# Optimization experiments

Measured on AMD Instinct MI355X. Metric: run time of the kernel, lower is better.

Reference implementation:

```python
import jax, jax.numpy as jnp
import numpy as np

B, S = 64, 100
N_EX, N_Q = 3000, 128
N_AT, N_IT = 1000, 1000
D_A = D_E = D_K = 128
GAMMA = 0.03


def _xavier(k, shape):
    lim = float(np.sqrt(6.0 / (shape[0] + shape[1])))
    return jax.random.uniform(k, shape, jnp.float32, -lim, lim)


def setup_inputs() -> dict:
    key = jax.random.key(0)
    ks = jax.random.split(key, 20)
    nq1 = N_Q + 1
    e_data = jax.random.randint(ks[0], (B, S), 0, N_EX, dtype=jnp.int32)
    a_data = jax.random.randint(ks[1], (B, S), 0, 2, dtype=jnp.int32)
    it_data = jax.random.randint(ks[2], (B, S), 0, N_IT, dtype=jnp.int32)
    at_data = jax.random.randint(ks[3], (B, S), 0, N_AT, dtype=jnp.int32)
    # binary Q-matrix with zeros replaced by gamma (as done in LPKT.__init__)
    q_bin = (jax.random.uniform(ks[4], (N_EX + 10, nq1)) < 0.05).astype(jnp.float32)
    q_matrix = jnp.where(q_bin > 0, 1.0, GAMMA)
    E_at = _xavier(ks[5], (N_AT + 10, D_K))
    E_it = _xavier(ks[6], (N_IT + 10, D_K))
    E_e = _xavier(ks[7], (N_EX + 10, D_E))
    h0 = _xavier(ks[8], (nq1, D_K))  # xavier-initialized initial skill state
    W1 = _xavier(ks[9], (D_A + D_E + D_K, D_K)); b1 = jnp.zeros(D_K, jnp.float32)
    W2 = _xavier(ks[10], (4 * D_K, D_K)); b2 = jnp.zeros(D_K, jnp.float32)
    W3 = _xavier(ks[11], (4 * D_K, D_K)); b3 = jnp.zeros(D_K, jnp.float32)
    W4 = _xavier(ks[12], (3 * D_K, D_K)); b4 = jnp.zeros(D_K, jnp.float32)
    W5 = _xavier(ks[13], (D_E + D_K, D_K)); b5 = jnp.zeros(D_K, jnp.float32)
    return dict(e_data=e_data, a_data=a_data, it_data=it_data, at_data=at_data,
                q_matrix=q_matrix, h0=h0, E_e=E_e, E_at=E_at, E_it=E_it,
                W1=W1, b1=b1, W2=W2, b2=b2, W3=W3, b3=b3, W4=W4, b4=b4, W5=W5, b5=b5)


def reference(e_data, a_data, it_data, at_data, q_matrix, h0, E_e, E_at, E_it,
              W1, b1, W2, b2, W3, b3, W4, b4, W5, b5):
    Bv, Sv = e_data.shape
    d_k = W2.shape[1]
    d_a = W1.shape[0] - E_e.shape[1] - d_k
    e_emb = E_e[e_data]            # (B,S,d_e)
    at_emb = E_at[at_data]         # (B,S,d_k)
    it_emb = E_it[it_data]         # (B,S,d_k)
    a_rep = jnp.broadcast_to(a_data.astype(jnp.float32)[..., None], (Bv, Sv, d_a))
    all_learning = jnp.concatenate([e_emb, at_emb, a_rep], 2) @ W1 + b1  # (B,S,d_k)
    q_all = q_matrix[e_data]       # (B,S,nq1)
    h_pre0 = jnp.broadcast_to(h0, (Bv,) + h0.shape)  # (B,nq1,d_k)
    q0 = q_all[:, 0]
    ht0 = jnp.einsum('bn,bnd->bd', q0, h_pre0) / q0.sum(1, keepdims=True)
    W4h, W4l, W4i = jnp.split(W4, 3, axis=0)

    def step(carry, x):
        learning_pre, h_pre, h_tilde_pre = carry
        q_e, q_next, it, learning, e_next = x
        feat = jnp.concatenate([learning_pre, it, learning, h_tilde_pre], 1)  # (B,4dk)
        lg = jnp.tanh(feat @ W2 + b2)
        gamma_l = jax.nn.sigmoid(feat @ W3 + b3)
        LG = gamma_l * (lg + 1.0) * 0.5                       # (B,d_k)
        LG_tilde = q_e[:, :, None] * LG[:, None, :]           # (B,nq1,d_k); dropout=eval identity
        gamma_f = jax.nn.sigmoid(jnp.einsum('bnd,df->bnf', h_pre, W4h)
                                 + (LG @ W4l + it @ W4i + b4)[:, None, :])
        h = LG_tilde + gamma_f * h_pre
        h_tilde = jnp.einsum('bn,bnd->bd', q_next, h) / q_next.sum(1, keepdims=True)
        y = jax.nn.sigmoid(jnp.concatenate([e_next, h_tilde], 1) @ W5 + b5).sum(1) / d_k
        return (learning, h, h_tilde), y

    xs = (jnp.swapaxes(q_all[:, :-1], 0, 1), jnp.swapaxes(q_all[:, 1:], 0, 1),
          jnp.swapaxes(it_emb[:, :-1], 0, 1), jnp.swapaxes(all_learning[:, :-1], 0, 1),
          jnp.swapaxes(e_emb[:, 1:], 0, 1))
    learning_pre0 = jnp.zeros((Bv, d_k), jnp.float32)
    _, ys = jax.lax.scan(step, (learning_pre0, h_pre0, ht0), xs)  # ys: (S-1,B)
    pred = jnp.zeros((Bv, Sv), jnp.float32).at[:, 1:].set(ys.T)
    return pred
```

## Files before the change

kernel.cpp:

```cpp
#include <hip/hip_runtime.h>
#include <hip/hip_fp16.h>
#include <math.h>


#define BB   64
#define SS   100
#define DK   128
#define NTH  512

#define OFF_PW1AB   0
#define OFF_PW23ABC 16384
#define OFF_PW4I    65536
#define OFF_PW5A    73728
#define OFF_PW23D   81920
#define OFF_PW4L    98304
#define OFF_AFRAG   114688
#define OFF_S1      122880
#define OFF_AL      123008
#define OFF_PRE     532608
#define OFF_HTV     2171008

typedef __attribute__((ext_vector_type(16))) float floatx16;
typedef __attribute__((ext_vector_type(8)))  short short8v;
typedef __attribute__((ext_vector_type(2)))  float floatx2;

__device__ __forceinline__ float frcp(float x) { return __builtin_amdgcn_rcpf(x); }
__device__ __forceinline__ float fsig(float x) { float t = __expf(-x); return frcp(1.0f + t); }
__device__ __forceinline__ float ftanh(float x) {
    x = fminf(20.0f, fmaxf(-20.0f, x));
    float t = __expf(-2.0f * x);
    return (1.0f - t) * frcp(1.0f + t);
}
__device__ __forceinline__ unsigned bfbits(float x) {
    unsigned u = __float_as_uint(x);
    return (u + 0x7fffu + ((u >> 16) & 1u)) >> 16;
}
__device__ __forceinline__ unsigned pack2(float a, float b) {
    return bfbits(a) | (bfbits(b) << 16);
}
__device__ __forceinline__ float blo(unsigned u) { return __uint_as_float(u << 16); }
__device__ __forceinline__ float bhi(unsigned u) { return __uint_as_float(u & 0xffff0000u); }

__device__ __forceinline__ unsigned cvtpk(float a, float b) {
    unsigned r;
    asm("v_cvt_pk_bf16_f32 %0, %1, %2" : "=v"(r) : "v"(a), "v"(b));
    return r;
}

__device__ __forceinline__ void wg_barrier() {
    asm volatile("s_waitcnt lgkmcnt(0)" ::: "memory");
    __builtin_amdgcn_s_barrier();
    asm volatile("" ::: "memory");
}

__global__ void k0_prep(const float* __restrict__ W1, const float* __restrict__ W2,
                        const float* __restrict__ W3, const float* __restrict__ W4,
                        const float* __restrict__ W5, unsigned* __restrict__ ws) {
    int g = blockIdx.x * blockDim.x + threadIdx.x;
    if (g < 16384) {
        int s = g >> 7, d = g & 127;
        ws[OFF_PW1AB + g] = pack2(W1[(2*s)*DK + d], W1[(2*s+1)*DK + d]);
    } else if (g < 65536) {
        int i = g - 16384; int s = i >> 8, j = i & 255;
        const float* M = (j < 128) ? W2 : W3; int jj = j & 127;
        ws[g] = pack2(M[(2*s)*DK + jj], M[(2*s+1)*DK + jj]);
    } else if (g < 73728) {
        int i = g - 65536; int s = i >> 7, j = i & 127;
        ws[g] = pack2(W4[(256+2*s)*DK + j], W4[(257+2*s)*DK + j]);
    } else if (g < 81920) {
        int i = g - 73728; int s = i >> 7, j = i & 127;
        ws[g] = pack2(W5[(2*s)*DK + j], W5[(2*s+1)*DK + j]);
    } else if (g < 98304) {
        int i = g - 81920;
        int q = i & 3, ln = (i >> 2) & 63, kb = (i >> 8) & 7, cw = i >> 11;
        int k = 16*kb + 8*(ln >> 5) + 2*q;
        int j = 32*cw + (ln & 31);
        const float* M = (j < 128) ? W2 : W3; int jj = j & 127;
        ws[g] = pack2(M[(384+k)*DK + jj], M[(385+k)*DK + jj]);
    } else if (g < 106496) {
        int i = g - 98304;
        int q = i & 3, ln = (i >> 2) & 63, kb = (i >> 8) & 7, cw = i >> 11;
        int k = 16*kb + 8*(ln >> 5) + 2*q;
        int j = 32*cw + (ln & 31);
        ws[g] = pack2(W4[(128+k)*DK + j], W4[(129+k)*DK + j]);
    } else if (g < 114688) {
    } else if (g < 122880) {
        int i = g - 114688;
        int gg = i >> 11, kb = (i >> 8) & 7, ln = (i >> 2) & 63, c = i & 3;
        int m = ln & 31, hp = ln >> 5;
        int k0 = 16*kb + 8*hp + 2*c;
        ws[g] = pack2(W4[k0*DK + 32*gg + m], W4[(k0+1)*DK + 32*gg + m]);
    } else if (g < 123008) {
        int d = g - 122880;
        float z = 0.f;
        for (int k = 0; k < 128; k++) z += W1[(256+k)*DK + d];
        ws[g] = __float_as_uint(z);
    }
}

__global__ __launch_bounds__(128)
void k1_al(const int* __restrict__ e_data, const int* __restrict__ a_data,
           const int* __restrict__ at_data, const float* __restrict__ Ee,
           const float* __restrict__ Eat, const float* __restrict__ b1,
           unsigned* __restrict__ ws) {
    const int b = blockIdx.x, t0 = 4 * blockIdx.y, tid = threadIdx.x;
    __shared__ __align__(16) float s_f[4][256];
    #pragma unroll
    for (int r = 0; r < 8; r++) {
        int id = r * 128 + tid; int i = id >> 8, k = id & 255;
        int t = t0 + i; float v = 0.f;
        if (t <= 98) {
            int e  = e_data[b*SS + t];
            int at = at_data[b*SS + t];
            v = (k < 128) ? Ee[(size_t)e*DK + k] : Eat[(size_t)at*DK + (k-128)];
        }
        s_f[i][k] = v;
    }
    __syncthreads();
    float s1v = __uint_as_float(ws[OFF_S1 + tid]);
    float b1v = b1[tid];
    float z[4];
    #pragma unroll
    for (int i = 0; i < 4; i++) z[i] = 0.f;
    #pragma unroll 2
    for (int s = 0; s < 128; s++) {
        unsigned w = ws[OFF_PW1AB + s*128 + tid];
        float wl = blo(w), wh = bhi(w);
        #pragma unroll
        for (int i = 0; i < 4; i++) {
            float2 f = *(const float2*)&s_f[i][2*s];
            z[i] += f.x*wl + f.y*wh;
        }
    }
    __half* AL = (__half*)(ws + OFF_AL);
    #pragma unroll
    for (int i = 0; i < 4; i++) {
        int t = t0 + i;
        if (t <= 98) {
            float a = (float)a_data[b*SS + t];
            AL[(size_t)(b*SS + t)*DK + tid] = __float2half(z[i] + a*s1v + b1v);
        }
    }
}

__global__ __launch_bounds__(512)
void k2_pre(const int* __restrict__ e_data, const int* __restrict__ it_data,
            const float* __restrict__ Eit, const float* __restrict__ Ee,
            const float* __restrict__ b2, const float* __restrict__ b3,
            const float* __restrict__ b4, const float* __restrict__ b5,
            unsigned* __restrict__ ws) {
    const int b = blockIdx.x, t0 = 4 * blockIdx.y, tid = threadIdx.x;
    __shared__ __align__(16) float s_g[4][384];
    __shared__ __align__(16) float s_e[4][128];
    const __half* AL = (const __half*)(ws + OFF_AL);
    #pragma unroll
    for (int r = 0; r < 3; r++) {
        int id = r * 512 + tid; int i = id / 384; int k = id - 384*i;
        int t = t0 + i; float v = 0.f;
        if (t <= 98) {
            if (k < 128)      v = (t == 0) ? 0.f : (float)AL[(size_t)(b*SS + t - 1)*DK + k];
            else if (k < 256) v = Eit[(size_t)it_data[b*SS + t]*DK + (k - 128)];
            else              v = (float)AL[(size_t)(b*SS + t)*DK + (k - 256)];
        }
        s_g[i][k] = v;
    }
    {
        int id = tid; int i = id >> 7, k = id & 127;
        int t = t0 + i;
        s_e[i][k] = (t <= 98) ? Ee[(size_t)e_data[b*SS + t + 1]*DK + k] : 0.f;
    }
    __syncthreads();
    __half* PRE = (__half*)(ws + OFF_PRE);
    float z[4];
    #pragma unroll
    for (int i = 0; i < 4; i++) z[i] = 0.f;
    int col; float bb;
    if (tid < 256) {
        int j = tid;
        #pragma unroll 2
        for (int s = 0; s < 192; s++) {
            unsigned w = ws[OFF_PW23ABC + s*256 + j];
            float wl = blo(w), wh = bhi(w);
            #pragma unroll
            for (int i = 0; i < 4; i++) {
                float2 f = *(const float2*)&s_g[i][2*s];
                z[i] += f.x*wl + f.y*wh;
            }
        }
        col = j; bb = (j < 128) ? b2[j] : b3[j - 128];
    } else if (tid < 384) {
        int j = tid - 256;
        #pragma unroll 2
        for (int s = 0; s < 64; s++) {
            unsigned w = ws[OFF_PW4I + s*128 + j];
            float wl = blo(w), wh = bhi(w);
            #pragma unroll
            for (int i = 0; i < 4; i++) {
                float2 f = *(const float2*)&s_g[i][128 + 2*s];
                z[i] += f.x*wl + f.y*wh;
            }
        }
        col = 256 + j; bb = b4[j];
    } else {
        int j = tid - 384;
        #pragma unroll 2
        for (int s = 0; s < 64; s++) {
            unsigned w = ws[OFF_PW5A + s*128 + j];
            float wl = blo(w), wh = bhi(w);
            #pragma unroll
            for (int i = 0; i < 4; i++) {
                float2 f = *(const float2*)&s_e[i][2*s];
                z[i] += f.x*wl + f.y*wh;
            }
        }
        col = 384 + j; bb = b5[j];
    }
    #pragma unroll
    for (int i = 0; i < 4; i++) {
        int t = t0 + i;
        if (t <= 98) PRE[(size_t)(b*SS + t)*512 + col] = __float2half(z[i] + bb);
    }
}

__global__ __launch_bounds__(NTH, 2)
void lpkt_kernel(const int* __restrict__ e_data, const float* __restrict__ qm,
                 const float* __restrict__ h0, unsigned* __restrict__ ws)
{
    const int b    = blockIdx.x;
    const int tid  = threadIdx.x;
    const int lane = tid & 63;
    const int w    = tid >> 6;
    const int g    = w & 3;
    const int hh   = w >> 2;
    const int h5   = lane >> 5;
    const int l31  = lane & 31;
    const int hf   = w >> 2;
    const int cw3  = w & 3;

    __shared__ __align__(16) unsigned s_frag[8192];
    __shared__ __align__(16) float s_big[2 * 128 * 34];
    __shared__ __align__(16) float s_pre[2][512];
    __shared__ __align__(16) float s_LG[128];
    __shared__ __align__(16) float s_h128[128];
    __shared__ __align__(16) float s_l128[2][128];
    __shared__ __align__(16) float s_red1[256];
    __shared__ __align__(16) float s_redE[256];
    __shared__ __align__(16) unsigned s_htvb[64];
    __shared__ __align__(16) float s_q[3][160];
    __shared__ int   s_ed[100];
    __shared__ float s_scal[2];

    uint4    afru[8], pw23b[8], pw4lb[4];
    floatx2  hreg2[2][8];
    floatx16 am[2];

    #pragma unroll
    for (int kb = 0; kb < 8; kb++)
        afru[kb] = ((const uint4*)(ws + OFF_AFRAG))[g*512 + kb*64 + lane];
    #pragma unroll
    for (int kb = 0; kb < 8; kb++)
        pw23b[kb] = ((const uint4*)(ws + OFF_PW23D))[(w*8 + kb)*64 + lane];
    #pragma unroll
    for (int kbl = 0; kbl < 4; kbl++)
        pw4lb[kbl] = ((const uint4*)(ws + OFF_PW4L))[((cw3*8 + hf*4 + kbl))*64 + lane];

    const __half* PRE = (const __half*)(ws + OFF_PRE);
    __half*       HTV = (__half*)(ws + OFF_HTV);

    if (tid < 100) s_ed[tid] = e_data[b*SS + tid];
    if (tid < 160) { s_q[0][tid] = 0.f; s_q[1][tid] = 0.f; s_q[2][tid] = 0.f; }
    if (tid < 129) {
        s_q[0][tid] = qm[(size_t)e_data[b*SS + 0]*129 + tid];
        s_q[1][tid] = qm[(size_t)e_data[b*SS + 1]*129 + tid];
    }
    s_pre[0][tid] = __half2float(PRE[(size_t)(b*SS)*512 + tid]);
    float  q_pf   = (tid < 129) ? qm[(size_t)e_data[b*SS + 2]*129 + tid] : 0.f;
    __half pre_pf = PRE[(size_t)(b*SS + 1)*512 + tid];

    #pragma unroll
    for (int i = 0; i < 2; i++) {
        const int cb = 2*hh + i;
        const int n = 32*cb + l31;
        #pragma unroll
        for (int m = 0; m < 8; m++) {
            int r = 2*m;
            int d = 32*g + (r&3) + 8*(r>>2) + 4*h5;
            hreg2[i][m] = *(const floatx2*)&h0[(size_t)n*DK + d];
        }
        #pragma unroll
        for (int q = 0; q < 4; q++) {
            int kb = 2*g + (q>>1);
            int lanep = l31 + ((q&1) << 5);
            int off = (((kb*4 + cb) << 10) + lanep*16 + (h5 << 3)) >> 2;
            uint2 pr = make_uint2(cvtpk(hreg2[i][2*q].x,   hreg2[i][2*q].y),
                                  cvtpk(hreg2[i][2*q+1].x, hreg2[i][2*q+1].y));
            *(uint2*)(s_frag + off) = pr;
        }
    }
    if (tid < 128) s_h128[tid] = h0[(size_t)128*DK + tid];
    __syncthreads();

    {
        if (w == 7) {
            float v0 = s_q[0][lane] + s_q[0][64+lane] + ((lane < 32) ? s_q[0][128+lane] : 0.f);
            float v1 = s_q[1][lane] + s_q[1][64+lane] + ((lane < 32) ? s_q[1][128+lane] : 0.f);
            #pragma unroll
            for (int m = 32; m > 0; m >>= 1) { v0 += __shfl_xor(v0, m); v1 += __shfl_xor(v1, m); }
            if (lane == 0) { s_scal[0] = v0; s_scal[1] = v1; }
        }
        floatx2 vv0[8];
        #pragma unroll
        for (int i = 0; i < 2; i++) {
            float qv = s_q[0][32*(2*hh + i) + l31];
            floatx2 qv2 = {qv, qv};
            #pragma unroll
            for (int m = 0; m < 8; m++) {
                if (i == 0) vv0[m] = qv2 * hreg2[i][m];
                else        vv0[m] = vv0[m] + qv2 * hreg2[i][m];
            }
        }
        #pragma unroll
        for (int m = 0; m < 8; m++) {
            int r = 2*m;
            int d = 32*g + (r&3) + 8*(r>>2) + 4*h5;
            s_big[(hh*128 + d)*34 + l31]       = vv0[m].x;
            s_big[(hh*128 + d + 1)*34 + l31]   = vv0[m].y;
        }
        #pragma unroll
        for (int i = 0; i < 2; i++) {
            const int cb = 2*hh + i;
            floatx16 a = (floatx16)(0.f);
            #pragma unroll
            for (int kb = 0; kb < 8; kb++) {
                short8v bf = *(const short8v*)((const char*)s_frag +
                               (((kb*4 + cb) << 10) + lane*16));
                a = __builtin_amdgcn_mfma_f32_32x32x16_bf16(
                        __builtin_bit_cast(short8v, afru[kb]), bf, a, 0, 0, 0);
            }
            am[i] = a;
        }
        {
            float part = 0.f;
            #pragma unroll
            for (int kbl = 0; kbl < 4; kbl++) {
                const int kb = 4*hh + kbl;
                const int kb0 = 16*kb + 8*h5;
                uint4 u = afru[kb];
                part += s_h128[kb0+0]*blo(u.x) + s_h128[kb0+1]*bhi(u.x);
                part += s_h128[kb0+2]*blo(u.y) + s_h128[kb0+3]*bhi(u.y);
                part += s_h128[kb0+4]*blo(u.z) + s_h128[kb0+5]*bhi(u.z);
                part += s_h128[kb0+6]*blo(u.w) + s_h128[kb0+7]*bhi(u.w);
            }
            part += __shfl_xor(part, 32);
            if (h5 == 0) s_l128[hh][32*g + l31] = part;
        }
    }
    __syncthreads();

    {
        const int row = 16*w + (lane >> 2);
        const int qr  = lane & 3;
        const float* basep = &s_big[(((qr >> 1) << 7) + row)*34 + ((qr & 1) << 4)];
        floatx2 a2 = {0.f, 0.f};
        #pragma unroll
        for (int jj = 0; jj < 8; jj++)
            a2 = a2 + *(const floatx2*)(basep + 2*jj);
        float a0 = a2.x + a2.y;
        a0 += __shfl_xor(a0, 1);
        a0 += __shfl_xor(a0, 2);
        float htvv = (a0 + s_q[0][128]*s_h128[row]) * frcp(s_scal[0]);
        float oth = __shfl_down(htvv, 4);
        if ((lane & 7) == 0) s_htvb[row >> 1] = cvtpk(htvv, oth);
    }
    __syncthreads();

    for (int t = 0; t < SS - 1; t++) {
        const int pbp = t & 1;
        const float* qc = s_q[t % 3];
        const float* qn = s_q[(t + 1) % 3];

        if (t + 2 <= 99 && tid < 129) s_q[(t + 2) % 3][tid] = q_pf;
        if (t + 1 <= 98)              s_pre[1 - pbp][tid] = __half2float(pre_pf);
        if (t + 3 <= 99 && tid < 129) q_pf  = qm[(size_t)s_ed[t + 3]*129 + tid];
        if (t + 2 <= 98)              pre_pf = PRE[(size_t)(b*SS + t + 2)*512 + tid];
        {
            floatx16 p1 = (floatx16)(0.f);
            #pragma unroll
            for (int kb = 0; kb < 8; kb++) {
                uint4 a1 = *(const uint4*)&s_htvb[kb*8 + 4*h5];
                p1 = __builtin_amdgcn_mfma_f32_32x32x16_bf16(
                        __builtin_bit_cast(short8v, a1),
                        __builtin_bit_cast(short8v, pw23b[kb]), p1, 0, 0, 0);
            }
            if (h5 == 0) s_red1[w*32 + l31] = p1[0];
        }
        wg_barrier();
        {
            const int m = 64*hf + lane;
            float z2v = s_red1[m]       + s_pre[pbp][m];
            float z3v = s_red1[128 + m] + s_pre[pbp][128 + m];
            float LGv = fsig(z3v) * (ftanh(z2v) + 1.f) * 0.5f;
            if (cw3 == 0) s_LG[m] = LGv;
            float oth = __shfl_xor(LGv, 1);
            float lo  = (lane & 1) ? oth : LGv;
            float hi  = (lane & 1) ? LGv : oth;
            int   pk  = (int)cvtpk(lo, hi);
            floatx16 p3 = (floatx16)(0.f);
            #pragma unroll
            for (int kbl = 0; kbl < 4; kbl++) {
                const int p0 = 8*kbl + 4*h5;
                uint4 a3;
                a3.x = (unsigned)__builtin_amdgcn_ds_bpermute(8*(p0+0), pk);
                a3.y = (unsigned)__builtin_amdgcn_ds_bpermute(8*(p0+1), pk);
                a3.z = (unsigned)__builtin_amdgcn_ds_bpermute(8*(p0+2), pk);
                a3.w = (unsigned)__builtin_amdgcn_ds_bpermute(8*(p0+3), pk);
                p3 = __builtin_amdgcn_mfma_f32_32x32x16_bf16(
                        __builtin_bit_cast(short8v, a3),
                        __builtin_bit_cast(short8v, pw4lb[kbl]), p3, 0, 0, 0);
            }
            if (h5 == 0) s_redE[hf*128 + 32*cw3 + l31] = p3[0];
        }
        wg_barrier();
        {
            floatx2 lg2[8], cv2[8], vv2[8];
            const float4* LG4 = (const float4*)s_LG;
            const float4* RE4 = (const float4*)s_redE;
            const float4* PR4 = (const float4*)s_pre[pbp];
            #pragma unroll
            for (int u = 0; u < 4; u++) {
                const int idx = 8*g + 2*u + h5;
                float4 lg = LG4[idx];
                float4 c0 = RE4[idx];
                float4 c1 = RE4[32 + idx];
                float4 pv = PR4[64 + idx];
                lg2[2*u]   = floatx2{lg.x, lg.y};
                lg2[2*u+1] = floatx2{lg.z, lg.w};
                cv2[2*u]   = floatx2{c0.x, c0.y} + floatx2{c1.x, c1.y} + floatx2{pv.x, pv.y};
                cv2[2*u+1] = floatx2{c0.z, c0.w} + floatx2{c1.z, c1.w} + floatx2{pv.z, pv.w};
            }
            const floatx2 nl2e2 = {-1.442695041f, -1.442695041f};
            #pragma unroll
            for (int i = 0; i < 2; i++) {
                const int cb = 2*hh + i;
                const int n = 32*cb + l31;
                const float qcv = qc[n], qnv = qn[n];
                const floatx2 qc2 = {qcv, qcv};
                const floatx2 qn2 = {qnv, qnv};
                #pragma unroll
                for (int m = 0; m < 8; m++) {
                    floatx2 x2 = floatx2{am[i][2*m], am[i][2*m+1]} + cv2[m];
                    floatx2 t2 = x2 * nl2e2;
                    floatx2 e2 = {__builtin_amdgcn_exp2f(t2.x), __builtin_amdgcn_exp2f(t2.y)};
                    floatx2 g2 = {frcp(1.f + e2.x), frcp(1.f + e2.y)};
                    floatx2 hn2 = qc2 * lg2[m] + g2 * hreg2[i][m];
                    hreg2[i][m] = hn2;
                    if (i == 0) vv2[m] = qn2 * hn2;
                    else        vv2[m] = vv2[m] + qn2 * hn2;
                }
            }
            #pragma unroll
            for (int i = 0; i < 2; i++) {
                const int cb = 2*hh + i;
                #pragma unroll
                for (int q = 0; q < 4; q++) {
                    int kb = 2*g + (q>>1);
                    int lanep = l31 + ((q&1) << 5);
                    int off = (((kb*4 + cb) << 10) + lanep*16 + (h5 << 3)) >> 2;
                    uint2 pr = make_uint2(cvtpk(hreg2[i][2*q].x,   hreg2[i][2*q].y),
                                          cvtpk(hreg2[i][2*q+1].x, hreg2[i][2*q+1].y));
                    *(uint2*)(s_frag + off) = pr;
                }
            }
            #pragma unroll
            for (int m = 0; m < 8; m++) {
                int r = 2*m;
                int d = 32*g + (r&3) + 8*(r>>2) + 4*h5;
                s_big[(hh*128 + d)*34 + l31]     = vv2[m].x;
                s_big[(hh*128 + d + 1)*34 + l31] = vv2[m].y;
            }
            if (tid < 128) {
                float c128 = s_redE[tid] + s_redE[128 + tid] + s_pre[pbp][256 + tid];
                float gg = fsig(s_l128[0][tid] + s_l128[1][tid] + c128);
                s_h128[tid] = qc[128]*s_LG[tid] + gg*s_h128[tid];
            }
        }
        wg_barrier();
        #pragma unroll
        for (int i = 0; i < 2; i++) {
            const int cb = 2*hh + i;
            floatx16 a = (floatx16)(0.f);
            #pragma unroll
            for (int kb = 0; kb < 8; kb++) {
                short8v bf = *(const short8v*)((const char*)s_frag +
                               (((kb*4 + cb) << 10) + lane*16));
                a = __builtin_amdgcn_mfma_f32_32x32x16_bf16(
                        __builtin_bit_cast(short8v, afru[kb]), bf, a, 0, 0, 0);
            }
            am[i] = a;
        }
        {
            float part = 0.f;
            #pragma unroll
            for (int kbl = 0; kbl < 4; kbl++) {
                const int kb = 4*hh + kbl;
                const int kb0 = 16*kb + 8*h5;
                uint4 u = afru[kb];
                part += s_h128[kb0+0]*blo(u.x) + s_h128[kb0+1]*bhi(u.x);
                part += s_h128[kb0+2]*blo(u.y) + s_h128[kb0+3]*bhi(u.y);
                part += s_h128[kb0+4]*blo(u.z) + s_h128[kb0+5]*bhi(u.z);
                part += s_h128[kb0+6]*blo(u.w) + s_h128[kb0+7]*bhi(u.w);
            }
            part += __shfl_xor(part, 32);
            if (h5 == 0) s_l128[hh][32*g + l31] = part;
        }
        if (w == 7 && t + 2 <= 99) {
            const float* q2 = s_q[(t + 2) % 3];
            float v = q2[lane] + q2[64 + lane] + ((lane < 32) ? q2[128 + lane] : 0.f);
            #pragma unroll
            for (int m = 32; m > 0; m >>= 1) v += __shfl_xor(v, m);
            if (lane == 0) s_scal[(t + 2) & 1] = v;
        }
        {
            const int row = 16*w + (lane >> 2);
            const int qr  = lane & 3;
            const float* basep = &s_big[(((qr >> 1) << 7) + row)*34 + ((qr & 1) << 4)];
            floatx2 a2 = {0.f, 0.f};
            #pragma unroll
            for (int jj = 0; jj < 8; jj++)
                a2 = a2 + *(const floatx2*)(basep + 2*jj);
            float a0 = a2.x + a2.y;
            a0 += __shfl_xor(a0, 1);
            a0 += __shfl_xor(a0, 2);
            float htvv = (a0 + qn[128]*s_h128[row]) * frcp(s_scal[(t + 1) & 1]);
            if ((lane & 3) == 0)
                HTV[((size_t)b*(SS-1) + t)*128 + row] = __float2half(htvv);
            float oth = __shfl_down(htvv, 4);
            if ((lane & 7) == 0) s_htvb[row >> 1] = cvtpk(htvv, oth);
        }
        wg_barrier();
    }
}

__global__ __launch_bounds__(128)
void k4_y(const float* __restrict__ W5, float* __restrict__ out,
          const unsigned* __restrict__ ws) {
    const int b = blockIdx.x, t = blockIdx.y, j = threadIdx.x;
    const __half* HTV = (const __half*)(ws + OFF_HTV);
    const __half* PRE = (const __half*)(ws + OFF_PRE);
    __shared__ float s_h[128];
    __shared__ float s_p[2];
    s_h[j] = __half2float(HTV[((size_t)b*(SS-1) + t)*128 + j]);
    __syncthreads();
    float z = __half2float(PRE[(size_t)(b*SS + t)*512 + 384 + j]);
    #pragma unroll 4
    for (int k = 0; k < 128; k++) z += s_h[k] * W5[(size_t)(128 + k)*DK + j];
    float v = fsig(z);
    #pragma unroll
    for (int m = 32; m > 0; m >>= 1) v += __shfl_xor(v, m);
    if ((j & 63) == 0) s_p[j >> 6] = v;
    __syncthreads();
    if (j == 0) {
        out[b*SS + t + 1] = (s_p[0] + s_p[1]) * (1.0f / 128.0f);
        if (t == 0) out[b*SS] = 0.f;
    }
}

extern "C" void kernel_launch(void* const* d_in, const int* in_sizes, int n_in,
                              void* d_out, int out_size, void* d_ws, size_t ws_size,
                              hipStream_t stream) {
    const int*   e_data  = (const int*)d_in[0];
    const int*   a_data  = (const int*)d_in[1];
    const int*   it_data = (const int*)d_in[2];
    const int*   at_data = (const int*)d_in[3];
    const float* qm  = (const float*)d_in[4];
    const float* h0  = (const float*)d_in[5];
    const float* Ee  = (const float*)d_in[6];
    const float* Eat = (const float*)d_in[7];
    const float* Eit = (const float*)d_in[8];
    const float* W1  = (const float*)d_in[9];
    const float* b1  = (const float*)d_in[10];
    const float* W2  = (const float*)d_in[11];
    const float* b2  = (const float*)d_in[12];
    const float* W3  = (const float*)d_in[13];
    const float* b3  = (const float*)d_in[14];
    const float* W4  = (const float*)d_in[15];
    const float* b4  = (const float*)d_in[16];
    const float* W5  = (const float*)d_in[17];
    const float* b5  = (const float*)d_in[18];
    float* out = (float*)d_out;
    unsigned* ws = (unsigned*)d_ws;

    k0_prep<<<dim3((123008 + 255) / 256), dim3(256), 0, stream>>>(W1, W2, W3, W4, W5, ws);
    k1_al<<<dim3(BB, 25), dim3(128), 0, stream>>>(e_data, a_data, at_data, Ee, Eat, b1, ws);
    k2_pre<<<dim3(BB, 25), dim3(512), 0, stream>>>(e_data, it_data, Eit, Ee, b2, b3, b4, b5, ws);
    lpkt_kernel<<<dim3(BB), dim3(NTH), 0, stream>>>(e_data, qm, h0, ws);
    k4_y<<<dim3(BB, SS - 1), dim3(128), 0, stream>>>(W5, out, ws);
}
```

Measured before the change: 644.7 us.

## Double recurrent-kernel workgroup to 1024 threads and split per-step work finer

The sequential scan kernel now launches 1024 threads per batch element instead of 512. Each wave handles one skill-column block instead of two, and the W2/W3 and W4 projections are split across more waves, with partial sums reduced through larger shared buffers. The precompute kernels also handle 8 timesteps per block instead of 4, so each weight load is reused more often. The aim is to shorten the latency-bound per-timestep critical path with more parallelism, at the cost of extra cross-wave reductions and heavier barriers across 16 waves. A W5 fragment pack is added in prep but appears unused.

```diff
diff --git a/kernel.cpp b/kernel.cpp
--- a/kernel.cpp
+++ b/kernel.cpp
@@ -6,7 +6,7 @@
 #define BB   64
 #define SS   100
 #define DK   128
-#define NTH  512
+#define NTH  1024
 
 #define OFF_PW1AB   0
 #define OFF_PW23ABC 16384
@@ -14,6 +14,7 @@
 #define OFF_PW5A    73728
 #define OFF_PW23D   81920
 #define OFF_PW4L    98304
+#define OFF_PW5B    106496
 #define OFF_AFRAG   114688
 #define OFF_S1      122880
 #define OFF_AL      123008
@@ -84,6 +85,11 @@
         int j = 32*cw + (ln & 31);
         ws[g] = pack2(W4[(128+k)*DK + j], W4[(129+k)*DK + j]);
     } else if (g < 114688) {
+        int i = g - 106496;
+        int q = i & 3, ln = (i >> 2) & 63, kb = (i >> 8) & 7, cw = i >> 11;
+        int k = 16*kb + 8*(ln >> 5) + 2*q;
+        int j = 32*cw + (ln & 31);
+        ws[g] = pack2(W5[(128+k)*DK + j], W5[(129+k)*DK + j]);
     } else if (g < 122880) {
         int i = g - 114688;
         int gg = i >> 11, kb = (i >> 8) & 7, ln = (i >> 2) & 63, c = i & 3;
@@ -103,10 +109,10 @@
            const int* __restrict__ at_data, const float* __restrict__ Ee,
            const float* __restrict__ Eat, const float* __restrict__ b1,
            unsigned* __restrict__ ws) {
-    const int b = blockIdx.x, t0 = 4 * blockIdx.y, tid = threadIdx.x;
-    __shared__ __align__(16) float s_f[4][256];
-    #pragma unroll
-    for (int r = 0; r < 8; r++) {
+    const int b = blockIdx.x, t0 = 8 * blockIdx.y, tid = threadIdx.x;
+    __shared__ __align__(16) float s_f[8][256];
+    #pragma unroll
+    for (int r = 0; r < 16; r++) {
         int id = r * 128 + tid; int i = id >> 8, k = id & 255;
         int t = t0 + i; float v = 0.f;
         if (t <= 98) {
@@ -119,22 +125,22 @@
     __syncthreads();
     float s1v = __uint_as_float(ws[OFF_S1 + tid]);
     float b1v = b1[tid];
-    float z[4];
-    #pragma unroll
-    for (int i = 0; i < 4; i++) z[i] = 0.f;
+    float z[8];
+    #pragma unroll
+    for (int i = 0; i < 8; i++) z[i] = 0.f;
     #pragma unroll 2
     for (int s = 0; s < 128; s++) {
         unsigned w = ws[OFF_PW1AB + s*128 + tid];
         float wl = blo(w), wh = bhi(w);
         #pragma unroll
-        for (int i = 0; i < 4; i++) {
+        for (int i = 0; i < 8; i++) {
             float2 f = *(const float2*)&s_f[i][2*s];
             z[i] += f.x*wl + f.y*wh;
         }
     }
     __half* AL = (__half*)(ws + OFF_AL);
     #pragma unroll
-    for (int i = 0; i < 4; i++) {
+    for (int i = 0; i < 8; i++) {
         int t = t0 + i;
         if (t <= 98) {
             float a = (float)a_data[b*SS + t];
@@ -149,12 +155,12 @@
             const float* __restrict__ b2, const float* __restrict__ b3,
             const float* __restrict__ b4, const float* __restrict__ b5,
             unsigned* __restrict__ ws) {
-    const int b = blockIdx.x, t0 = 4 * blockIdx.y, tid = threadIdx.x;
-    __shared__ __align__(16) float s_g[4][384];
-    __shared__ __align__(16) float s_e[4][128];
+    const int b = blockIdx.x, t0 = 8 * blockIdx.y, tid = threadIdx.x;
+    __shared__ __align__(16) float s_g[8][384];
+    __shared__ __align__(16) float s_e[8][128];
     const __half* AL = (const __half*)(ws + OFF_AL);
     #pragma unroll
-    for (int r = 0; r < 3; r++) {
+    for (int r = 0; r < 6; r++) {
         int id = r * 512 + tid; int i = id / 384; int k = id - 384*i;
         int t = t0 + i; float v = 0.f;
         if (t <= 98) {
@@ -164,16 +170,17 @@
         }
         s_g[i][k] = v;
     }
-    {
-        int id = tid; int i = id >> 7, k = id & 127;
+    #pragma unroll
+    for (int r = 0; r < 2; r++) {
+        int id = r * 512 + tid; int i = id >> 7, k = id & 127;
         int t = t0 + i;
         s_e[i][k] = (t <= 98) ? Ee[(size_t)e_data[b*SS + t + 1]*DK + k] : 0.f;
     }
     __syncthreads();
     __half* PRE = (__half*)(ws + OFF_PRE);
-    float z[4];
-    #pragma unroll
-    for (int i = 0; i < 4; i++) z[i] = 0.f;
+    float z[8];
+    #pragma unroll
+    for (int i = 0; i < 8; i++) z[i] = 0.f;
     int col; float bb;
     if (tid < 256) {
         int j = tid;
@@ -182,7 +189,7 @@
             unsigned w = ws[OFF_PW23ABC + s*256 + j];
             float wl = blo(w), wh = bhi(w);
             #pragma unroll
-            for (int i = 0; i < 4; i++) {
+            for (int i = 0; i < 8; i++) {
                 float2 f = *(const float2*)&s_g[i][2*s];
                 z[i] += f.x*wl + f.y*wh;
             }
@@ -195,7 +202,7 @@
             unsigned w = ws[OFF_PW4I + s*128 + j];
             float wl = blo(w), wh = bhi(w);
             #pragma unroll
-            for (int i = 0; i < 4; i++) {
+            for (int i = 0; i < 8; i++) {
                 float2 f = *(const float2*)&s_g[i][128 + 2*s];
                 z[i] += f.x*wl + f.y*wh;
             }
@@ -208,7 +215,7 @@
             unsigned w = ws[OFF_PW5A + s*128 + j];
             float wl = blo(w), wh = bhi(w);
             #pragma unroll
-            for (int i = 0; i < 4; i++) {
+            for (int i = 0; i < 8; i++) {
                 float2 f = *(const float2*)&s_e[i][2*s];
                 z[i] += f.x*wl + f.y*wh;
             }
@@ -216,13 +223,13 @@
         col = 384 + j; bb = b5[j];
     }
     #pragma unroll
-    for (int i = 0; i < 4; i++) {
+    for (int i = 0; i < 8; i++) {
         int t = t0 + i;
         if (t <= 98) PRE[(size_t)(b*SS + t)*512 + col] = __float2half(z[i] + bb);
     }
 }
 
-__global__ __launch_bounds__(NTH, 2)
+__global__ __launch_bounds__(NTH, 1)
 void lpkt_kernel(const int* __restrict__ e_data, const float* __restrict__ qm,
                  const float* __restrict__ h0, unsigned* __restrict__ ws)
 {
@@ -230,39 +237,39 @@
     const int tid  = threadIdx.x;
     const int lane = tid & 63;
     const int w    = tid >> 6;
-    const int g    = w & 3;
-    const int hh   = w >> 2;
     const int h5   = lane >> 5;
     const int l31  = lane & 31;
-    const int hf   = w >> 2;
-    const int cw3  = w & 3;
+    const int g    = w & 3;
+    const int cb   = w >> 2;
+    const int c1   = w & 7;
+    const int kh1  = w >> 3;
 
     __shared__ __align__(16) unsigned s_frag[8192];
-    __shared__ __align__(16) float s_big[2 * 128 * 34];
+    __shared__ __align__(16) float s_big[2 * 128 * 66];
     __shared__ __align__(16) float s_pre[2][512];
     __shared__ __align__(16) float s_LG[128];
     __shared__ __align__(16) float s_h128[128];
-    __shared__ __align__(16) float s_l128[2][128];
-    __shared__ __align__(16) float s_red1[256];
-    __shared__ __align__(16) float s_redE[256];
+    __shared__ __align__(16) float s_l128[4][128];
+    __shared__ __align__(16) float s_red1[512];
+    __shared__ __align__(16) float s_redE[512];
     __shared__ __align__(16) unsigned s_htvb[64];
     __shared__ __align__(16) float s_q[3][160];
     __shared__ int   s_ed[100];
     __shared__ float s_scal[2];
 
-    uint4    afru[8], pw23b[8], pw4lb[4];
-    floatx2  hreg2[2][8];
-    floatx16 am[2];
+    uint4    afru[8], pw23bh[4], pw4lb2[2];
+    floatx2  hreg2[8];
+    floatx16 am;
 
     #pragma unroll
     for (int kb = 0; kb < 8; kb++)
         afru[kb] = ((const uint4*)(ws + OFF_AFRAG))[g*512 + kb*64 + lane];
     #pragma unroll
-    for (int kb = 0; kb < 8; kb++)
-        pw23b[kb] = ((const uint4*)(ws + OFF_PW23D))[(w*8 + kb)*64 + lane];
-    #pragma unroll
     for (int kbl = 0; kbl < 4; kbl++)
-        pw4lb[kbl] = ((const uint4*)(ws + OFF_PW4L))[((cw3*8 + hf*4 + kbl))*64 + lane];
+        pw23bh[kbl] = ((const uint4*)(ws + OFF_PW23D))[(c1*8 + 4*kh1 + kbl)*64 + lane];
+    #pragma unroll
+    for (int kbl = 0; kbl < 2; kbl++)
+        pw4lb2[kbl] = ((const uint4*)(ws + OFF_PW4L))[(g*8 + 2*cb + kbl)*64 + lane];
 
     const __half* PRE = (const __half*)(ws + OFF_PRE);
     __half*       HTV = (__half*)(ws + OFF_HTV);
@@ -273,27 +280,25 @@
         s_q[0][tid] = qm[(size_t)e_data[b*SS + 0]*129 + tid];
         s_q[1][tid] = qm[(size_t)e_data[b*SS + 1]*129 + tid];
     }
-    s_pre[0][tid] = __half2float(PRE[(size_t)(b*SS)*512 + tid]);
+    if (tid < 512) s_pre[0][tid] = __half2float(PRE[(size_t)(b*SS)*512 + tid]);
     float  q_pf   = (tid < 129) ? qm[(size_t)e_data[b*SS + 2]*129 + tid] : 0.f;
-    __half pre_pf = PRE[(size_t)(b*SS + 1)*512 + tid];
-
-    #pragma unroll
-    for (int i = 0; i < 2; i++) {
-        const int cb = 2*hh + i;
+    __half pre_pf = (tid < 512) ? PRE[(size_t)(b*SS + 1)*512 + tid] : __half(0.f);
+
+    {
         const int n = 32*cb + l31;
         #pragma unroll
         for (int m = 0; m < 8; m++) {
             int r = 2*m;
             int d = 32*g + (r&3) + 8*(r>>2) + 4*h5;
-            hreg2[i][m] = *(const floatx2*)&h0[(size_t)n*DK + d];
+            hreg2[m] = *(const floatx2*)&h0[(size_t)n*DK + d];
         }
         #pragma unroll
         for (int q = 0; q < 4; q++) {
             int kb = 2*g + (q>>1);
             int lanep = l31 + ((q&1) << 5);
             int off = (((kb*4 + cb) << 10) + lanep*16 + (h5 << 3)) >> 2;
-            uint2 pr = make_uint2(cvtpk(hreg2[i][2*q].x,   hreg2[i][2*q].y),
-                                  cvtpk(hreg2[i][2*q+1].x, hreg2[i][2*q+1].y));
+            uint2 pr = make_uint2(cvtpk(hreg2[2*q].x,   hreg2[2*q].y),
+                                  cvtpk(hreg2[2*q+1].x, hreg2[2*q+1].y));
             *(uint2*)(s_frag + off) = pr;
         }
     }
@@ -301,34 +306,24 @@
     __syncthreads();
 
     {
-        if (w == 7) {
+        if (w == 15) {
             float v0 = s_q[0][lane] + s_q[0][64+lane] + ((lane < 32) ? s_q[0][128+lane] : 0.f);
             float v1 = s_q[1][lane] + s_q[1][64+lane] + ((lane < 32) ? s_q[1][128+lane] : 0.f);
             #pragma unroll
             for (int m = 32; m > 0; m >>= 1) { v0 += __shfl_xor(v0, m); v1 += __shfl_xor(v1, m); }
             if (lane == 0) { s_scal[0] = v0; s_scal[1] = v1; }
         }
-        floatx2 vv0[8];
-        #pragma unroll
-        for (int i = 0; i < 2; i++) {
-            float qv = s_q[0][32*(2*hh + i) + l31];
-            floatx2 qv2 = {qv, qv};
-            #pragma unroll
-            for (int m = 0; m < 8; m++) {
-                if (i == 0) vv0[m] = qv2 * hreg2[i][m];
-                else        vv0[m] = vv0[m] + qv2 * hreg2[i][m];
-            }
-        }
+        const int n = 32*cb + l31;
+        const float qv = s_q[0][n];
+        const int half = cb >> 1, colc = 32*(cb & 1) + l31;
         #pragma unroll
         for (int m = 0; m < 8; m++) {
             int r = 2*m;
             int d = 32*g + (r&3) + 8*(r>>2) + 4*h5;
-            s_big[(hh*128 + d)*34 + l31]       = vv0[m].x;
-            s_big[(hh*128 + d + 1)*34 + l31]   = vv0[m].y;
-        }
-        #pragma unroll
-        for (int i = 0; i < 2; i++) {
-            const int cb = 2*hh + i;
+            s_big[((half*128) + d)*66 + colc]     = qv * hreg2[m].x;
+            s_big[((half*128) + d + 1)*66 + colc] = qv * hreg2[m].y;
+        }
+        {
             floatx16 a = (floatx16)(0.f);
             #pragma unroll
             for (int kb = 0; kb < 8; kb++) {
@@ -337,13 +332,13 @@
                 a = __builtin_amdgcn_mfma_f32_32x32x16_bf16(
                         __builtin_bit_cast(short8v, afru[kb]), bf, a, 0, 0, 0);
             }
-            am[i] = a;
+            am = a;
         }
         {
             float part = 0.f;
             #pragma unroll
-            for (int kbl = 0; kbl < 4; kbl++) {
-                const int kb = 4*hh + kbl;
+            for (int kbl = 0; kbl < 2; kbl++) {
+                const int kb = 2*cb + kbl;
                 const int kb0 = 16*kb + 8*h5;
                 uint4 u = afru[kb];
                 part += s_h128[kb0+0]*blo(u.x) + s_h128[kb0+1]*bhi(u.x);
@@ -352,15 +347,15 @@
                 part += s_h128[kb0+6]*blo(u.w) + s_h128[kb0+7]*bhi(u.w);
             }
             part += __shfl_xor(part, 32);
-            if (h5 == 0) s_l128[hh][32*g + l31] = part;
+            if (h5 == 0) s_l128[cb][32*g + l31] = part;
         }
     }
     __syncthreads();
 
     {
-        const int row = 16*w + (lane >> 2);
-        const int qr  = lane & 3;
-        const float* basep = &s_big[(((qr >> 1) << 7) + row)*34 + ((qr & 1) << 4)];
+        const int row = 8*w + (lane >> 3);
+        const int sub = lane & 7;
+        const float* basep = &s_big[(((sub >> 2) << 7) + row)*66 + ((sub & 3) << 4)];
         floatx2 a2 = {0.f, 0.f};
         #pragma unroll
         for (int jj = 0; jj < 8; jj++)
@@ -368,9 +363,10 @@
         float a0 = a2.x + a2.y;
         a0 += __shfl_xor(a0, 1);
         a0 += __shfl_xor(a0, 2);
+        a0 += __shfl_xor(a0, 4);
         float htvv = (a0 + s_q[0][128]*s_h128[row]) * frcp(s_scal[0]);
-        float oth = __shfl_down(htvv, 4);
-        if ((lane & 7) == 0) s_htvb[row >> 1] = cvtpk(htvv, oth);
+        float oth = __shfl_down(htvv, 8);
+        if ((lane & 15) == 0) s_htvb[row >> 1] = cvtpk(htvv, oth);
     }
     __syncthreads();
 
@@ -380,114 +376,120 @@
         const float* qn = s_q[(t + 1) % 3];
 
         if (t + 2 <= 99 && tid < 129) s_q[(t + 2) % 3][tid] = q_pf;
-        if (t + 1 <= 98)              s_pre[1 - pbp][tid] = __half2float(pre_pf);
+        if (t + 1 <= 98 && tid < 512) s_pre[1 - pbp][tid] = __half2float(pre_pf);
         if (t + 3 <= 99 && tid < 129) q_pf  = qm[(size_t)s_ed[t + 3]*129 + tid];
-        if (t + 2 <= 98)              pre_pf = PRE[(size_t)(b*SS + t + 2)*512 + tid];
+        if (t + 2 <= 98 && tid < 512) pre_pf = PRE[(size_t)(b*SS + t + 2)*512 + tid];
         {
             floatx16 p1 = (floatx16)(0.f);
             #pragma unroll
-            for (int kb = 0; kb < 8; kb++) {
+            for (int kbl = 0; kbl < 4; kbl++) {
+                const int kb = 4*kh1 + kbl;
                 uint4 a1 = *(const uint4*)&s_htvb[kb*8 + 4*h5];
                 p1 = __builtin_amdgcn_mfma_f32_32x32x16_bf16(
                         __builtin_bit_cast(short8v, a1),
-                        __builtin_bit_cast(short8v, pw23b[kb]), p1, 0, 0, 0);
-            }
-            if (h5 == 0) s_red1[w*32 + l31] = p1[0];
+                        __builtin_bit_cast(short8v, pw23bh[kbl]), p1, 0, 0, 0);
+            }
+            if (h5 == 0) s_red1[kh1*256 + 32*c1 + l31] = p1[0];
         }
         wg_barrier();
         {
-            const int m = 64*hf + lane;
-            float z2v = s_red1[m]       + s_pre[pbp][m];
-            float z3v = s_red1[128 + m] + s_pre[pbp][128 + m];
+            const int m = 32*cb + l31;
+            float z2v = s_red1[m]       + s_red1[256 + m] + s_pre[pbp][m];
+            float z3v = s_red1[128 + m] + s_red1[384 + m] + s_pre[pbp][128 + m];
             float LGv = fsig(z3v) * (ftanh(z2v) + 1.f) * 0.5f;
-            if (cw3 == 0) s_LG[m] = LGv;
+            if (g == 0 && h5 == 0) s_LG[m] = LGv;
             float oth = __shfl_xor(LGv, 1);
             float lo  = (lane & 1) ? oth : LGv;
             float hi  = (lane & 1) ? LGv : oth;
             int   pk  = (int)cvtpk(lo, hi);
             floatx16 p3 = (floatx16)(0.f);
             #pragma unroll
-            for (int kbl = 0; kbl < 4; kbl++) {
+            for (int kbl = 0; kbl < 2; kbl++) {
                 const int p0 = 8*kbl + 4*h5;
                 uint4 a3;
-                a3.x = (unsigned)__builtin_amdgcn_ds_bpermute(8*(p0+0), pk);
-                a3.y = (unsigned)__builtin_amdgcn_ds_bpermute(8*(p0+1), pk);
-                a3.z = (unsigned)__builtin_amdgcn_ds_bpermute(8*(p0+2), pk);
-                a3.w = (unsigned)__builtin_amdgcn_ds_bpermute(8*(p0+3), pk);
+                a3.x = (unsigned)__builtin_amdgcn_ds_bpermute(8*(2*(p0+0)), pk);
+                a3.y = (unsigned)__builtin_amdgcn_ds_bpermute(8*(2*(p0+1)), pk);
+                a3.z = (unsigned)__builtin_amdgcn_ds_bpermute(8*(2*(p0+2)), pk);
+                a3.w = (unsigned)__builtin_amdgcn_ds_bpermute(8*(2*(p0+3)), pk);
                 p3 = __builtin_amdgcn_mfma_f32_32x32x16_bf16(
                         __builtin_bit_cast(short8v, a3),
-                        __builtin_bit_cast(short8v, pw4lb[kbl]), p3, 0, 0, 0);
-            }
-            if (h5 == 0) s_redE[hf*128 + 32*cw3 + l31] = p3[0];
+                        __builtin_bit_cast(short8v, pw4lb2[kbl]), p3, 0, 0, 0);
+            }
+            if (h5 == 0) s_redE[cb*128 + 32*g + l31] = p3[0];
         }
         wg_barrier();
         {
-            floatx2 lg2[8], cv2[8], vv2[8];
             const float4* LG4 = (const float4*)s_LG;
             const float4* RE4 = (const float4*)s_redE;
             const float4* PR4 = (const float4*)s_pre[pbp];
+            const int n = 32*cb + l31;
+            const float qcv = qc[n], qnv = qn[n];
+            const floatx2 qc2 = {qcv, qcv};
+            const floatx2 qn2 = {qnv, qnv};
+            const floatx2 nl2e2 = {-1.442695041f, -1.442695041f};
+            floatx2 vv2[8];
             #pragma unroll
             for (int u = 0; u < 4; u++) {
                 const int idx = 8*g + 2*u + h5;
-                float4 lg = LG4[idx];
-                float4 c0 = RE4[idx];
-                float4 c1 = RE4[32 + idx];
-                float4 pv = PR4[64 + idx];
-                lg2[2*u]   = floatx2{lg.x, lg.y};
-                lg2[2*u+1] = floatx2{lg.z, lg.w};
-                cv2[2*u]   = floatx2{c0.x, c0.y} + floatx2{c1.x, c1.y} + floatx2{pv.x, pv.y};
-                cv2[2*u+1] = floatx2{c0.z, c0.w} + floatx2{c1.z, c1.w} + floatx2{pv.z, pv.w};
-            }
-            const floatx2 nl2e2 = {-1.442695041f, -1.442695041f};
-            #pragma unroll
-            for (int i = 0; i < 2; i++) {
-                const int cb = 2*hh + i;
-                const int n = 32*cb + l31;
-                const float qcv = qc[n], qnv = qn[n];
-                const floatx2 qc2 = {qcv, qcv};
-                const floatx2 qn2 = {qnv, qnv};
-                #pragma unroll
-                for (int m = 0; m < 8; m++) {
-                    floatx2 x2 = floatx2{am[i][2*m], am[i][2*m+1]} + cv2[m];
+                float4 lg  = LG4[idx];
+                float4 e0  = RE4[idx];
+                float4 e1  = RE4[32 + idx];
+                float4 e2v = RE4[64 + idx];
+                float4 e3  = RE4[96 + idx];
+                float4 pv  = PR4[64 + idx];
+                floatx2 lgA = {lg.x, lg.y}, lgB = {lg.z, lg.w};
+                floatx2 cvA = {e0.x + e1.x + e2v.x + e3.x + pv.x,
+                               e0.y + e1.y + e2v.y + e3.y + pv.y};
+                floatx2 cvB = {e0.z + e1.z + e2v.z + e3.z + pv.z,
+                               e0.w + e1.w + e2v.w + e3.w + pv.w};
+                {
+                    const int m = 2*u;
+                    floatx2 x2 = floatx2{am[2*m], am[2*m+1]} + cvA;
                     floatx2 t2 = x2 * nl2e2;
-                    floatx2 e2 = {__builtin_amdgcn_exp2f(t2.x), __builtin_amdgcn_exp2f(t2.y)};
-                    floatx2 g2 = {frcp(1.f + e2.x), frcp(1.f + e2.y)};
-                    floatx2 hn2 = qc2 * lg2[m] + g2 * hreg2[i][m];
-                    hreg2[i][m] = hn2;
-                    if (i == 0) vv2[m] = qn2 * hn2;
-                    else        vv2[m] = vv2[m] + qn2 * hn2;
+                    floatx2 ex = {__builtin_amdgcn_exp2f(t2.x), __builtin_amdgcn_exp2f(t2.y)};
+                    floatx2 g2 = {frcp(1.f + ex.x), frcp(1.f + ex.y)};
+                    floatx2 hn = qc2 * lgA + g2 * hreg2[m];
+                    hreg2[m] = hn;
+                    vv2[m] = qn2 * hn;
                 }
-            }
-            #pragma unroll
-            for (int i = 0; i < 2; i++) {
-                const int cb = 2*hh + i;
-                #pragma unroll
-                for (int q = 0; q < 4; q++) {
-                    int kb = 2*g + (q>>1);
-                    int lanep = l31 + ((q&1) << 5);
-                    int off = (((kb*4 + cb) << 10) + lanep*16 + (h5 << 3)) >> 2;
-                    uint2 pr = make_uint2(cvtpk(hreg2[i][2*q].x,   hreg2[i][2*q].y),
-                                          cvtpk(hreg2[i][2*q+1].x, hreg2[i][2*q+1].y));
-                    *(uint2*)(s_frag + off) = pr;
+                {
+                    const int m = 2*u + 1;
+                    floatx2 x2 = floatx2{am[2*m], am[2*m+1]} + cvB;
+                    floatx2 t2 = x2 * nl2e2;
+                    floatx2 ex = {__builtin_amdgcn_exp2f(t2.x), __builtin_amdgcn_exp2f(t2.y)};
+                    floatx2 g2 = {frcp(1.f + ex.x), frcp(1.f + ex.y)};
+                    floatx2 hn = qc2 * lgB + g2 * hreg2[m];
+                    hreg2[m] = hn;
+                    vv2[m] = qn2 * hn;
                 }
             }
+            #pragma unroll
+            for (int q = 0; q < 4; q++) {
+                int kb = 2*g + (q>>1);
+                int lanep = l31 + ((q&1) << 5);
+                int off = (((kb*4 + cb) << 10) + lanep*16 + (h5 << 3)) >> 2;
+                uint2 pr = make_uint2(cvtpk(hreg2[2*q].x,   hreg2[2*q].y),
+                                      cvtpk(hreg2[2*q+1].x, hreg2[2*q+1].y));
+                *(uint2*)(s_frag + off) = pr;
+            }
+            const int half = cb >> 1, colc = 32*(cb & 1) + l31;
             #pragma unroll
             for (int m = 0; m < 8; m++) {
                 int r = 2*m;
                 int d = 32*g + (r&3) + 8*(r>>2) + 4*h5;
-                s_big[(hh*128 + d)*34 + l31]     = vv2[m].x;
-                s_big[(hh*128 + d + 1)*34 + l31] = vv2[m].y;
+                s_big[((half*128) + d)*66 + colc]     = vv2[m].x;
+                s_big[((half*128) + d + 1)*66 + colc] = vv2[m].y;
             }
             if (tid < 128) {
-                float c128 = s_redE[tid] + s_redE[128 + tid] + s_pre[pbp][256 + tid];
-                float gg = fsig(s_l128[0][tid] + s_l128[1][tid] + c128);
+                float c128 = s_redE[tid] + s_redE[128 + tid] + s_redE[256 + tid]
+                           + s_redE[384 + tid] + s_pre[pbp][256 + tid];
+                float ll = s_l128[0][tid] + s_l128[1][tid] + s_l128[2][tid] + s_l128[3][tid];
+                float gg = fsig(ll + c128);
                 s_h128[tid] = qc[128]*s_LG[tid] + gg*s_h128[tid];
             }
         }
         wg_barrier();
-        #pragma unroll
-        for (int i = 0; i < 2; i++) {
-            const int cb = 2*hh + i;
+        {
             floatx16 a = (floatx16)(0.f);
             #pragma unroll
             for (int kb = 0; kb < 8; kb++) {
@@ -496,13 +498,13 @@
                 a = __builtin_amdgcn_mfma_f32_32x32x16_bf16(
                         __builtin_bit_cast(short8v, afru[kb]), bf, a, 0, 0, 0);
             }
-            am[i] = a;
+            am = a;
         }
         {
             float part = 0.f;
             #pragma unroll
-            for (int kbl = 0; kbl < 4; kbl++) {
-                const int kb = 4*hh + kbl;
+            for (int kbl = 0; kbl < 2; kbl++) {
+                const int kb = 2*cb + kbl;
                 const int kb0 = 16*kb + 8*h5;
                 uint4 u = afru[kb];
                 part += s_h128[kb0+0]*blo(u.x) + s_h128[kb0+1]*bhi(u.x);
@@ -511,9 +513,9 @@
                 part += s_h128[kb0+6]*blo(u.w) + s_h128[kb0+7]*bhi(u.w);
             }
             part += __shfl_xor(part, 32);
-            if (h5 == 0) s_l128[hh][32*g + l31] = part;
-        }
-        if (w == 7 && t + 2 <= 99) {
+            if (h5 == 0) s_l128[cb][32*g + l31] = part;
+        }
+        if (w == 15 && t + 2 <= 99) {
             const float* q2 = s_q[(t + 2) % 3];
             float v = q2[lane] + q2[64 + lane] + ((lane < 32) ? q2[128 + lane] : 0.f);
             #pragma unroll
@@ -521,9 +523,9 @@
             if (lane == 0) s_scal[(t + 2) & 1] = v;
         }
         {
-            const int row = 16*w + (lane >> 2);
-            const int qr  = lane & 3;
-            const float* basep = &s_big[(((qr >> 1) << 7) + row)*34 + ((qr & 1) << 4)];
+            const int row = 8*w + (lane >> 3);
+            const int sub = lane & 7;
+            const float* basep = &s_big[(((sub >> 2) << 7) + row)*66 + ((sub & 3) << 4)];
             floatx2 a2 = {0.f, 0.f};
             #pragma unroll
             for (int jj = 0; jj < 8; jj++)
@@ -531,11 +533,12 @@
             float a0 = a2.x + a2.y;
             a0 += __shfl_xor(a0, 1);
             a0 += __shfl_xor(a0, 2);
+            a0 += __shfl_xor(a0, 4);
             float htvv = (a0 + qn[128]*s_h128[row]) * frcp(s_scal[(t + 1) & 1]);
-            if ((lane & 3) == 0)
+            if ((lane & 7) == 0)
                 HTV[((size_t)b*(SS-1) + t)*128 + row] = __float2half(htvv);
-            float oth = __shfl_down(htvv, 4);
-            if ((lane & 7) == 0) s_htvb[row >> 1] = cvtpk(htvv, oth);
+            float oth = __shfl_down(htvv, 8);
+            if ((lane & 15) == 0) s_htvb[row >> 1] = cvtpk(htvv, oth);
         }
         wg_barrier();
     }
@@ -591,8 +594,8 @@
     unsigned* ws = (unsigned*)d_ws;
 
     k0_prep<<<dim3((123008 + 255) / 256), dim3(256), 0, stream>>>(W1, W2, W3, W4, W5, ws);
-    k1_al<<<dim3(BB, 25), dim3(128), 0, stream>>>(e_data, a_data, at_data, Ee, Eat, b1, ws);
-    k2_pre<<<dim3(BB, 25), dim3(512), 0, stream>>>(e_data, it_data, Eit, Ee, b2, b3, b4, b5, ws);
+    k1_al<<<dim3(BB, 13), dim3(128), 0, stream>>>(e_data, a_data, at_data, Ee, Eat, b1, ws);
+    k2_pre<<<dim3(BB, 13), dim3(512), 0, stream>>>(e_data, it_data, Eit, Ee, b2, b3, b4, b5, ws);
     lpkt_kernel<<<dim3(BB), dim3(NTH), 0, stream>>>(e_data, qm, h0, ws);
     k4_y<<<dim3(BB, SS - 1), dim3(128), 0, stream>>>(W5, out, ws);
 }
```

Measured after the change: 1.113 ms. +72.6%, slower.
